# Performance work log

Measured on AMD Instinct MI355X. Metric: run time of the kernel, lower is better.

The kernel has to match this reference:

```python
import jax, jax.numpy as jnp
import numpy as np

DIM_H = 384
EPS = 0.5
HID = 768
NN = 3   # num_normal_labels (B,I,O)
NL = 7   # num_labels (O, B/I x POS/NEG/NEU)


def _make_w_trans():
    # ote_vocab: B=0, I=1, O=2 ; ts_vocab: O=0, B-POS=1, B-NEG=2, B-NEU=3, I-POS=4, I-NEG=5, I-NEU=6
    W = np.zeros((NN, NL), dtype=np.float32)
    W[0, 1] = W[0, 2] = W[0, 3] = 1.0 / 3.0  # B -> B-*
    W[1, 4] = W[1, 5] = W[1, 6] = 1.0 / 3.0  # I -> I-*
    W[2, 0] = 1.0                            # O -> O
    return jnp.asarray(W)


def setup_inputs() -> dict:
    key = jax.random.key(0)
    ks = jax.random.split(key, 16)
    B, S = 32, 512
    s = 0.02
    inp = {
        'x': jax.random.normal(ks[0], (B, S, HID), jnp.float32),
        'attention_mask': jnp.ones((B, S), jnp.int32),
        'labels': jax.random.randint(ks[1], (B, S), 0, NL, jnp.int32),
        'labels_normal': jax.random.randint(ks[2], (B, S), 0, NN, jnp.int32),
        'W_fc_normal': jax.random.normal(ks[3], (HID, NN), jnp.float32) * s,
        'b_fc_normal': jnp.zeros((NN,), jnp.float32),
        'w_ih_f': jax.random.normal(ks[4], (4 * DIM_H, HID), jnp.float32) * s,
        'w_hh_f': jax.random.normal(ks[5], (4 * DIM_H, DIM_H), jnp.float32) * s,
        'b_f': jnp.zeros((4 * DIM_H,), jnp.float32),
        'w_ih_b': jax.random.normal(ks[6], (4 * DIM_H, HID), jnp.float32) * s,
        'w_hh_b': jax.random.normal(ks[7], (4 * DIM_H, DIM_H), jnp.float32) * s,
        'b_b': jnp.zeros((4 * DIM_H,), jnp.float32),
        'W_gate': jax.random.uniform(ks[8], (2 * DIM_H, 2 * DIM_H), jnp.float32, -0.2, 0.2),
        'W_fc_upper': jax.random.normal(ks[9], (2 * DIM_H, NL), jnp.float32) * s,
        'b_fc_upper': jnp.zeros((NL,), jnp.float32),
        'W_trans': _make_w_trans(),
    }
    return inp


def _lstm_dir(xs, w_ih, w_hh, b):
    # xs: [S, B, HID] time-major; PyTorch gate order i,f,g,o
    B = xs.shape[1]
    pre = jnp.einsum('sbh,gh->sbg', xs, w_ih) + b  # precompute input projections

    def step(carry, p_t):
        h, c = carry
        g = p_t + h @ w_hh.T
        i, f, gg, o = jnp.split(g, 4, axis=-1)
        c = jax.nn.sigmoid(f) * c + jax.nn.sigmoid(i) * jnp.tanh(gg)
        h = jax.nn.sigmoid(o) * jnp.tanh(c)
        return (h, c), h

    init = (jnp.zeros((B, DIM_H), xs.dtype), jnp.zeros((B, DIM_H), xs.dtype))
    _, hs = jax.lax.scan(step, init, pre)
    return hs  # [S, B, DIM_H]


def _masked_ce(logits, labels, mask):
    logp = jax.nn.log_softmax(logits, axis=-1)
    nll = -jnp.take_along_axis(logp, labels[..., None].astype(jnp.int32), axis=-1)[..., 0]
    m = mask.astype(logits.dtype)
    return jnp.sum(nll * m) / jnp.sum(m)


def reference(x, attention_mask, labels, labels_normal, W_fc_normal, b_fc_normal,
              w_ih_f, w_hh_f, b_f, w_ih_b, w_hh_b, b_b, W_gate,
              W_fc_upper, b_fc_upper, W_trans):
    z_t = x @ W_fc_normal + b_fc_normal                      # [B,S,NN]
    loss = _masked_ce(z_t, labels_normal, attention_mask)

    xs = jnp.transpose(x, (1, 0, 2))                         # [S,B,HID]
    hf = _lstm_dir(xs, w_ih_f, w_hh_f, b_f)
    hb = _lstm_dir(xs[::-1], w_ih_b, w_hh_b, b_b)[::-1]
    h_s = jnp.concatenate([hf, hb], axis=-1)                 # [S,B,2*DIM_H]

    # gated highway recurrence: gates depend only on h_s -> batched matmul + linear scan
    g = jax.nn.sigmoid(h_s @ W_gate)                         # [S,B,768]

    def gate_step(h_prev, inp):
        ht, gt = inp
        h = gt * ht + (1.0 - gt) * h_prev
        return h, h

    _, rest = jax.lax.scan(gate_step, h_s[0], (h_s[1:], g[1:]))
    h_tilde = jnp.concatenate([h_s[:1], rest], axis=0)       # [S,B,768]
    h_tilde = jnp.transpose(h_tilde, (1, 0, 2))              # [B,S,768]; dropout = identity (eval)

    z_s = h_tilde @ W_fc_upper + b_fc_upper                  # [B,S,NL]
    p = jax.nn.softmax(z_t, axis=-1)
    alpha = EPS * jnp.sum(p * p, axis=-1, keepdims=True)     # [B,S,1]
    z_s_prime = z_t @ W_trans                                # [B,S,NL]
    z_s_tilde = z_s_prime * alpha + z_s * (1.0 - alpha)

    loss = loss + _masked_ce(z_s_tilde, labels, attention_mask)
    return loss, z_s_tilde
```

## Files before the change

kernel.cpp:

```cpp
#include <hip/hip_runtime.h>

#define B_SZ   32
#define S_LEN  512
#define HID    768
#define DH     384
#define G4     1536
#define NPOS   16384
#define EPS_C  0.5f
#define NCH    24576
#define CHK    64
#define NCHK   8

typedef _Float16 h2 __attribute__((ext_vector_type(2)));
typedef short bf16x8 __attribute__((ext_vector_type(8)));
typedef float f32x4 __attribute__((ext_vector_type(4)));

static __device__ __forceinline__ float sigm(float x) { return 1.0f / (1.0f + __expf(-x)); }
static __device__ __forceinline__ float tanh_fast(float x) {
    return 1.0f - 2.0f / (__expf(2.0f * x) + 1.0f);
}

static __device__ __forceinline__ unsigned short f2bf(float f) {
    union { float f; unsigned u; } v; v.f = f;
    unsigned r = v.u + 0x7FFF + ((v.u >> 16) & 1);
    return (unsigned short)(r >> 16);
}
static __device__ __forceinline__ float bf2f(unsigned short u) {
    union { unsigned u; float f; } v; v.u = ((unsigned)u) << 16; return v.f;
}

static __device__ __forceinline__ float wred(float v) {
#pragma unroll
    for (int off = 32; off > 0; off >>= 1) v += __shfl_down(v, off, 64);
    return v;
}

static __device__ __forceinline__ float dot2acc(h2 a, h2 b, float c) {
#if __has_builtin(__builtin_amdgcn_fdot2)
    return __builtin_amdgcn_fdot2(a, b, c, false);
#else
    return c + (float)a.x * (float)b.x + (float)a.y * (float)b.y;
#endif
}

static __device__ __forceinline__ h2 hcast(unsigned u) { return __builtin_bit_cast(h2, u); }

template <int CTRL>
static __device__ __forceinline__ float qperm_add(float v) {
#if __has_builtin(__builtin_amdgcn_mov_dpp)
    int o = __builtin_amdgcn_mov_dpp(__builtin_bit_cast(int, v), CTRL, 0xF, 0xF, true);
    return v + __builtin_bit_cast(float, o);
#else
    return v + __shfl_xor(v, (CTRL == 0xB1) ? 1 : 2, 64);
#endif
}

__global__ void wprep(const float* __restrict__ wf, const float* __restrict__ wb,
                      unsigned* __restrict__ wpk) {
    int gid = blockIdx.x * 256 + threadIdx.x;
    int d = (gid >= 294912) ? 1 : 0;
    int j = gid - d * 294912;
    const float* src = d ? wb : wf;
    _Float16 a = (_Float16)src[2 * j];
    _Float16 b = (_Float16)src[2 * j + 1];
    unsigned pa = __builtin_bit_cast(unsigned short, a);
    unsigned pb = __builtin_bit_cast(unsigned short, b);
    wpk[(size_t)d * 294912 + j] = pa | (pb << 16);
}

__global__ __launch_bounds__(256) void cast_bf16(
    const float* __restrict__ src, unsigned short* __restrict__ dst, int n4) {
    int i = blockIdx.x * 256 + threadIdx.x;
    if (i >= n4) return;
    float4 v = *(const float4*)(src + (size_t)i * 4);
    ushort4 o;
    o.x = f2bf(v.x); o.y = f2bf(v.y); o.z = f2bf(v.z); o.w = f2bf(v.w);
    *(ushort4*)(dst + (size_t)i * 4) = o;
}

__global__ __launch_bounds__(256) void wgt_prep(
    const float* __restrict__ Wg, unsigned short* __restrict__ Wgt) {
    int i = blockIdx.x * 256 + threadIdx.x;
    int k = i / 768, n = i - k * 768;
    Wgt[(size_t)n * 768 + k] = f2bf(Wg[i]);
}

__global__ __launch_bounds__(256) void zt_kernel(
    const float* __restrict__ x, const int* __restrict__ amask,
    const int* __restrict__ labn, const float* __restrict__ Wfc,
    const float* __restrict__ bfc, const float* __restrict__ Wtr,
    float* __restrict__ alpha, float* __restrict__ zsp,
    float* __restrict__ p0, float* __restrict__ p2) {
    const int gid  = blockIdx.x * blockDim.x + threadIdx.x;
    const int pos  = gid >> 6, lane = gid & 63, wv = threadIdx.x >> 6;
    __shared__ float r0[4], r2[4];
    const float* xp = x + (size_t)pos * HID;
    float a0 = 0.f, a1 = 0.f, a2 = 0.f;
#pragma unroll
    for (int j = 0; j < 12; ++j) {
        int k = lane + (j << 6);
        float xv = xp[k];
        a0 += xv * Wfc[k * 3 + 0];
        a1 += xv * Wfc[k * 3 + 1];
        a2 += xv * Wfc[k * 3 + 2];
    }
    a0 = wred(a0); a1 = wred(a1); a2 = wred(a2);
    if (lane == 0) {
        float z0 = a0 + bfc[0], z1 = a1 + bfc[1], z2 = a2 + bfc[2];
        float mx = fmaxf(z0, fmaxf(z1, z2));
        float e0 = __expf(z0 - mx), e1 = __expf(z1 - mx), e2 = __expf(z2 - mx);
        float se = e0 + e1 + e2;
        float m  = (float)amask[pos];
        int  lab = labn[pos];
        float zl = (lab == 0) ? z0 : ((lab == 1) ? z1 : z2);
        r0[wv] = (mx + __logf(se) - zl) * m;
        r2[wv] = m;
        float q0 = e0 / se, q1 = e1 / se, q2 = e2 / se;
        alpha[pos] = EPS_C * (q0 * q0 + q1 * q1 + q2 * q2);
#pragma unroll
        for (int cc = 0; cc < 7; ++cc)
            zsp[(size_t)pos * 7 + cc] = z0 * Wtr[cc] + z1 * Wtr[7 + cc] + z2 * Wtr[14 + cc];
    }
    __syncthreads();
    if (threadIdx.x == 0) {
        p0[blockIdx.x] = r0[0] + r0[1] + r0[2] + r0[3];
        p2[blockIdx.x] = r2[0] + r2[1] + r2[2] + r2[3];
    }
}

__global__ __launch_bounds__(256) void gemm_mfma(
    const unsigned short* __restrict__ A, const unsigned short* __restrict__ B,
    const float* __restrict__ bias, void* __restrict__ Cout,
    int M, int N, int K, int mode) {
    __shared__ __align__(16) unsigned short As[128][40];
    __shared__ __align__(16) unsigned short Bs[128][40];
    const int tid = threadIdx.x;
    const int m0 = blockIdx.y * 128, n0 = blockIdx.x * 128;
    const int wave = tid >> 6, lane = tid & 63;
    const int wm = (wave & 1) * 64, wn = (wave >> 1) * 64;
    const int lm = lane & 15, quad = lane >> 4;
    f32x4 acc[4][4] = {};

    for (int k0 = 0; k0 < K; k0 += 32) {
#pragma unroll
        for (int r = 0; r < 2; ++r) {
            int seg = tid + r * 256;
            int row = seg >> 2, c16 = (seg & 3) << 3;
            uint4 va = *(const uint4*)(A + (size_t)(m0 + row) * K + k0 + c16);
            *(uint4*)&As[row][c16] = va;
            uint4 vb = *(const uint4*)(B + (size_t)(n0 + row) * K + k0 + c16);
            *(uint4*)&Bs[row][c16] = vb;
        }
        __syncthreads();
        bf16x8 af[4], bfr[4];
#pragma unroll
        for (int i = 0; i < 4; ++i) {
            af[i]  = *(const bf16x8*)&As[wm + i * 16 + lm][quad * 8];
            bfr[i] = *(const bf16x8*)&Bs[wn + i * 16 + lm][quad * 8];
        }
#pragma unroll
        for (int mi = 0; mi < 4; ++mi)
#pragma unroll
            for (int ni = 0; ni < 4; ++ni)
                acc[mi][ni] = __builtin_amdgcn_mfma_f32_16x16x32_bf16(
                    af[mi], bfr[ni], acc[mi][ni], 0, 0, 0);
        __syncthreads();
    }

    const int rbase = quad * 4;
#pragma unroll
    for (int mi = 0; mi < 4; ++mi) {
#pragma unroll
        for (int ni = 0; ni < 4; ++ni) {
            const int col = n0 + wn + ni * 16 + lm;
            const float bv = (mode == 0) ? bias[col] : 0.0f;
#pragma unroll
            for (int r = 0; r < 4; ++r) {
                const int row = m0 + wm + mi * 16 + rbase + r;
                float v = acc[mi][ni][r];
                if (mode == 0)
                    ((unsigned short*)Cout)[(size_t)row * N + col] = f2bf(v + bv);
                else
                    ((unsigned short*)Cout)[(size_t)row * N + col] = f2bf(sigm(v));
            }
        }
    }
}

#define DOT8(W, H, A0, A1) { \
    A0 = dot2acc(hcast(W.x), hcast(H.x), A0); \
    A1 = dot2acc(hcast(W.y), hcast(H.y), A1); \
    A0 = dot2acc(hcast(W.z), hcast(H.z), A0); \
    A1 = dot2acc(hcast(W.w), hcast(H.w), A1); }

__global__ __launch_bounds__(768)
__attribute__((amdgpu_waves_per_eu(3, 3)))
void lstm_scan9(
    const unsigned* __restrict__ wpk,
    const unsigned short* __restrict__ pre,
    unsigned short* __restrict__ h_sb,
    unsigned long long* __restrict__ hx64) {
    const int blk   = blockIdx.x;
    const int chain = blk & 63;
    const int rp    = blk >> 6;
    const int d = chain >> 5, b = chain & 31;
    const int tid = threadIdx.x;
    const int j = tid >> 2;
    const int p = tid & 3;
    const int ga = j / 96, ua = j - ga * 96;
    const int base = rp * 96;
    const int Ga = ga * 384 + base + ua;

    __shared__ __align__(16) _Float16 lh16[2][384];
    __shared__ float    lpreV[384];
    __shared__ unsigned lpreT[384];

    const uint4* wqA = (const uint4*)wpk + ((size_t)d * 1536 + Ga) * 48 + p * 12;
    const uint4* wqB = wqA + 36864;
    const uint4 wa0 = wqA[0], wa1 = wqA[1], wa2  = wqA[2],  wa3  = wqA[3],
                wa4 = wqA[4], wa5 = wqA[5], wa6  = wqA[6],  wa7  = wqA[7],
                wa8 = wqA[8], wa9 = wqA[9], wa10 = wqA[10], wa11 = wqA[11];
    const uint4 wb0 = wqB[0], wb1 = wqB[1], wb2  = wqB[2],  wb3  = wqB[3],
                wb4 = wqB[4], wb5 = wqB[5], wb6  = wqB[6],  wb7  = wqB[7],
                wb8 = wqB[8], wb9 = wqB[9], wb10 = wqB[10], wb11 = wqB[11];

    const unsigned short* prb =
        pre + ((size_t)d * B_SZ + b) * S_LEN * G4 + Ga + ((p == 1) ? 768 : 0);

    float c = 0.0f;

    for (int s = 0; s < S_LEN; ++s) {
        const int t  = d ? (S_LEN - 1 - s) : s;
        const int lb = s & 1;
        float prev = 0.0f;
        if (p < 2) prev = bf2f(prb[(size_t)t * G4]);

        if (s == 0) {
            if (tid < 384) { lh16[0][tid] = (_Float16)0.0f; lpreT[tid] = 0xFFFFFFFFu; }
        } else if (tid < 288) {
            const int uu = tid + (tid >= base ? 96 : 0);
            const unsigned long long* srcp =
                hx64 + ((size_t)((s - 1) & 1) * 64 + chain) * 384 + uu;
            unsigned long long v =
                __hip_atomic_load(srcp, __ATOMIC_RELAXED, __HIP_MEMORY_SCOPE_AGENT);
            while ((unsigned)(v >> 32) != (unsigned)(s - 1)) {
                __builtin_amdgcn_s_sleep(1);
                v = __hip_atomic_load(srcp, __ATOMIC_RELAXED, __HIP_MEMORY_SCOPE_AGENT);
            }
            lh16[lb][uu] = (_Float16)__builtin_bit_cast(float, (unsigned)v);
        }
        __syncthreads();

        {
            const uint4* hq = (const uint4*)&lh16[lb][0] + p * 12;
            const uint4 hv0 = hq[0], hv1 = hq[1], hv2  = hq[2],  hv3  = hq[3],
                        hv4 = hq[4], hv5 = hq[5], hv6  = hq[6],  hv7  = hq[7],
                        hv8 = hq[8], hv9 = hq[9], hv10 = hq[10], hv11 = hq[11];
            float a0 = 0.f, a1 = 0.f, b0 = 0.f, b1 = 0.f;
            DOT8(wa0, hv0, a0, a1)  DOT8(wa1, hv1, a0, a1)  DOT8(wa2,  hv2,  a0, a1)
            DOT8(wa3, hv3, a0, a1)  DOT8(wa4, hv4, a0, a1)  DOT8(wa5,  hv5,  a0, a1)
            DOT8(wa6, hv6, a0, a1)  DOT8(wa7, hv7, a0, a1)  DOT8(wa8,  hv8,  a0, a1)
            DOT8(wa9, hv9, a0, a1)  DOT8(wa10, hv10, a0, a1) DOT8(wa11, hv11, a0, a1)
            DOT8(wb0, hv0, b0, b1)  DOT8(wb1, hv1, b0, b1)  DOT8(wb2,  hv2,  b0, b1)
            DOT8(wb3, hv3, b0, b1)  DOT8(wb4, hv4, b0, b1)  DOT8(wb5,  hv5,  b0, b1)
            DOT8(wb6, hv6, b0, b1)  DOT8(wb7, hv7, b0, b1)  DOT8(wb8,  hv8,  b0, b1)
            DOT8(wb9, hv9, b0, b1)  DOT8(wb10, hv10, b0, b1) DOT8(wb11, hv11, b0, b1)
            float sa = a0 + a1, sb = b0 + b1;
            sa = qperm_add<0xB1>(sa); sa = qperm_add<0x4E>(sa);
            sb = qperm_add<0xB1>(sb); sb = qperm_add<0x4E>(sb);
            if (p == 0) {
                lpreV[j] = sa + prev;
                __hip_atomic_store(&lpreT[j], (unsigned)s, __ATOMIC_RELEASE,
                                   __HIP_MEMORY_SCOPE_WORKGROUP);
            } else if (p == 1) {
                lpreV[j + 192] = sb + prev;
                __hip_atomic_store(&lpreT[j + 192], (unsigned)s, __ATOMIC_RELEASE,
                                   __HIP_MEMORY_SCOPE_WORKGROUP);
            }
        }

        if (tid < 96) {
            const unsigned sv = (unsigned)s;
#pragma unroll
            for (int jj = 0; jj < 4; ++jj) {
                unsigned* tp = &lpreT[jj * 96 + tid];
                while (__hip_atomic_load(tp, __ATOMIC_ACQUIRE,
                                         __HIP_MEMORY_SCOPE_WORKGROUP) != sv) {}
            }
            float gi = lpreV[tid], gf = lpreV[96 + tid];
            float gg = lpreV[192 + tid], go = lpreV[288 + tid];
            c = sigm(gf) * c + sigm(gi) * tanh_fast(gg);
            float h = sigm(go) * tanh_fast(c);
            unsigned long long v = ((unsigned long long)sv << 32)
                                 | (unsigned long long)__builtin_bit_cast(unsigned, h);
            __hip_atomic_store(hx64 + ((size_t)lb * 64 + chain) * 384 + base + tid,
                               v, __ATOMIC_RELAXED, __HIP_MEMORY_SCOPE_AGENT);
            h_sb[((size_t)t * B_SZ + b) * HID + d * DH + base + tid] = f2bf(h);
            lh16[lb ^ 1][base + tid] = (_Float16)h;
        }
    }
}

__global__ __launch_bounds__(256) void gscanA(
    const unsigned short* __restrict__ g, const unsigned short* __restrict__ hsb,
    float2* __restrict__ ab) {
    int id = blockIdx.x * 256 + threadIdx.x;
    int chunk = id / NCH, chain = id - chunk * NCH;
    int t0 = chunk * CHK;
    float A = 1.f, Bv = 0.f;
    for (int i = 0; i < CHK; ++i) {
        int t = t0 + i;
        size_t idx = (size_t)t * NCH + chain;
        float gv = bf2f(g[idx]);
        float hv = bf2f(hsb[idx]);
        float a = (t == 0) ? 0.f : (1.f - gv);
        float bb = (t == 0) ? hv : gv * hv;
        A  = a * A;
        Bv = a * Bv + bb;
    }
    ab[id] = make_float2(A, Bv);
}

__global__ __launch_bounds__(256) void gscanB(
    const float2* __restrict__ ab, float* __restrict__ cin) {
    int chain = blockIdx.x * 256 + threadIdx.x;
    float h = 0.f;
#pragma unroll
    for (int j = 0; j < NCHK; ++j) {
        cin[(size_t)j * NCH + chain] = h;
        float2 t = ab[(size_t)j * NCH + chain];
        h = t.x * h + t.y;
    }
}

__global__ __launch_bounds__(256) void gscanC(
    const unsigned short* __restrict__ g, unsigned short* __restrict__ hsb,
    const float* __restrict__ cin) {
    int id = blockIdx.x * 256 + threadIdx.x;
    int chunk = id / NCH, chain = id - chunk * NCH;
    int t0 = chunk * CHK;
    float h = cin[(size_t)chunk * NCH + chain];
    for (int i = 0; i < CHK; ++i) {
        int t = t0 + i;
        size_t idx = (size_t)t * NCH + chain;
        float gv = bf2f(g[idx]);
        float v  = bf2f(hsb[idx]);
        h = (t == 0) ? v : (gv * v + (1.f - gv) * h);
        hsb[idx] = f2bf(h);
    }
}

__global__ __launch_bounds__(256) void final_k(
    const unsigned short* __restrict__ ht, const float* __restrict__ Wup,
    const float* __restrict__ bup, const float* __restrict__ alpha,
    const float* __restrict__ zsp, const int* __restrict__ labels,
    const int* __restrict__ amask, float* __restrict__ out, float* __restrict__ p1) {
    const int gid = blockIdx.x * blockDim.x + threadIdx.x;
    const int pos = gid >> 6, lane = gid & 63, wv = threadIdx.x >> 6;
    __shared__ float r1[4];
    const int bb = pos >> 9, tt = pos & 511;
    const unsigned short* hp = ht + (size_t)tt * (B_SZ * HID) + (size_t)bb * HID;
    float acc[7] = {};
#pragma unroll
    for (int j = 0; j < 12; ++j) {
        int k = lane + (j << 6);
        float hv = bf2f(hp[k]);
        const float* wr = Wup + k * 7;
#pragma unroll
        for (int cc = 0; cc < 7; ++cc) acc[cc] += hv * wr[cc];
    }
#pragma unroll
    for (int cc = 0; cc < 7; ++cc) acc[cc] = wred(acc[cc]);
    if (lane == 0) {
        float al = alpha[pos];
        float z[7], mx = -1e30f;
#pragma unroll
        for (int cc = 0; cc < 7; ++cc) {
            float v = acc[cc] + bup[cc];
            v = zsp[(size_t)pos * 7 + cc] * al + v * (1.0f - al);
            z[cc] = v;
            mx = fmaxf(mx, v);
            out[1 + (size_t)pos * 7 + cc] = v;
        }
        float se = 0.f;
#pragma unroll
        for (int cc = 0; cc < 7; ++cc) se += __expf(z[cc] - mx);
        float lse = mx + __logf(se);
        int lab = labels[pos];
        float zl = z[0];
#pragma unroll
        for (int cc = 1; cc < 7; ++cc) if (lab == cc) zl = z[cc];
        float m = (float)amask[pos];
        r1[wv] = (lse - zl) * m;
    }
    __syncthreads();
    if (threadIdx.x == 0)
        p1[blockIdx.x] = r1[0] + r1[1] + r1[2] + r1[3];
}

__global__ __launch_bounds__(256) void loss_k(
    const float* __restrict__ p0, const float* __restrict__ p1,
    const float* __restrict__ p2, float* __restrict__ out) {
    const int tid = threadIdx.x, lane = tid & 63, wv = tid >> 6;
    __shared__ float rs[4][3];
    float s0 = 0.f, s1 = 0.f, s2 = 0.f;
    for (int i = tid; i < 4096; i += 256) {
        s0 += p0[i]; s1 += p1[i]; s2 += p2[i];
    }
    s0 = wred(s0); s1 = wred(s1); s2 = wred(s2);
    if (lane == 0) { rs[wv][0] = s0; rs[wv][1] = s1; rs[wv][2] = s2; }
    __syncthreads();
    if (tid == 0) {
        float t0 = rs[0][0] + rs[1][0] + rs[2][0] + rs[3][0];
        float t1 = rs[0][1] + rs[1][1] + rs[2][1] + rs[3][1];
        float t2 = rs[0][2] + rs[1][2] + rs[2][2] + rs[3][2];
        out[0] = t0 / t2 + t1 / t2;
    }
}

extern "C" void kernel_launch(void* const* d_in, const int* in_sizes, int n_in,
                              void* d_out, int out_size, void* d_ws, size_t ws_size,
                              hipStream_t stream) {
    const float* x     = (const float*)d_in[0];
    const int*   amask = (const int*)d_in[1];
    const int*   labels= (const int*)d_in[2];
    const int*   labn  = (const int*)d_in[3];
    const float* Wfc   = (const float*)d_in[4];
    const float* bfc   = (const float*)d_in[5];
    const float* wihf  = (const float*)d_in[6];
    const float* whhf  = (const float*)d_in[7];
    const float* bf    = (const float*)d_in[8];
    const float* wihb  = (const float*)d_in[9];
    const float* whhb  = (const float*)d_in[10];
    const float* bb    = (const float*)d_in[11];
    const float* Wg    = (const float*)d_in[12];
    const float* Wup   = (const float*)d_in[13];
    const float* bup   = (const float*)d_in[14];
    const float* Wtr   = (const float*)d_in[15];
    float* out = (float*)d_out;
    (void)in_sizes; (void)n_in; (void)out_size; (void)ws_size;

    char* ws = (char*)d_ws;
    size_t off = 0;
    auto alloc = [&](size_t bytes) -> char* {
        char* p = ws + off;
        off = (off + bytes + 255) & ~(size_t)255;
        return p;
    };
    unsigned* w16buf    = (unsigned*)alloc((size_t)2 * 1536 * 192 * 4);
    unsigned short* pre = (unsigned short*)alloc((size_t)2 * NPOS * G4 * 2);
    unsigned short* xb  = (unsigned short*)alloc((size_t)NPOS * HID * 2);
    unsigned short* wfb = (unsigned short*)alloc((size_t)G4 * HID * 2);
    unsigned short* wbb = (unsigned short*)alloc((size_t)G4 * HID * 2);
    unsigned short* wgt = (unsigned short*)alloc((size_t)HID * HID * 2);
    float* alpha        = (float*)alloc((size_t)NPOS * 4);
    float* zsp          = (float*)alloc((size_t)NPOS * 7 * 4);
    unsigned long long* hx64 = (unsigned long long*)alloc((size_t)2 * 64 * 384 * 8);
    float2* ab          = (float2*)alloc((size_t)NCHK * NCH * 8);
    float* cin          = (float*)alloc((size_t)NCHK * NCH * 4);
    float* part0        = (float*)alloc(4096 * 4);
    float* part1        = (float*)alloc(4096 * 4);
    float* part2        = (float*)alloc(4096 * 4);
    unsigned short* gbuf = (unsigned short*)pre;
    unsigned short* h_sb = xb;


    wprep<<<2304, 256, 0, stream>>>(whhf, whhb, w16buf);
    cast_bf16<<<12288, 256, 0, stream>>>(x, xb, NPOS * HID / 4);
    cast_bf16<<<1152, 256, 0, stream>>>(wihf, wfb, G4 * HID / 4);
    cast_bf16<<<1152, 256, 0, stream>>>(wihb, wbb, G4 * HID / 4);
    wgt_prep<<<2304, 256, 0, stream>>>(Wg, wgt);

    zt_kernel<<<4096, 256, 0, stream>>>(x, amask, labn, Wfc, bfc, Wtr, alpha, zsp,
                                        part0, part2);

    gemm_mfma<<<dim3(12, 128), 256, 0, stream>>>(xb, wfb, bf, pre, NPOS, G4, HID, 0);
    gemm_mfma<<<dim3(12, 128), 256, 0, stream>>>(xb, wbb, bb, pre + (size_t)NPOS * G4,
                                                 NPOS, G4, HID, 0);

    lstm_scan9<<<256, 768, 0, stream>>>(w16buf, pre, h_sb, hx64);

    gemm_mfma<<<dim3(6, 128), 256, 0, stream>>>(h_sb, wgt, nullptr, gbuf, NPOS, HID, HID, 1);

    gscanA<<<768, 256, 0, stream>>>(gbuf, h_sb, ab);
    gscanB<<<96, 256, 0, stream>>>(ab, cin);
    gscanC<<<768, 256, 0, stream>>>(gbuf, h_sb, cin);

    final_k<<<4096, 256, 0, stream>>>(h_sb, Wup, bup, alpha, zsp, labels, amask, out, part1);

    loss_k<<<1, 256, 0, stream>>>(part0, part1, part2, out);
}
```

Measured before the change: 1.368 ms.

## Give each hidden unit all four gates in one 8-lane group, removing LDS handoff

The LSTM scan kernel now assigns 8 lanes per hidden unit, with each lane computing partial dot products for all four gates (i,f,g,o) over a 48-element slice of h. The lanes reduce with DPP shifts, and lane 0 applies the cell update directly. This removes the shared-memory gate staging and the intra-workgroup spin-wait flags that the 96 update threads used. Each lane now loads four weight slices instead of two. The DPP row-shift reduction must stay correct within 8-lane groups, and the fallback path uses shfl_down.

```diff
diff --git a/kernel.cpp b/kernel.cpp
--- a/kernel.cpp
+++ b/kernel.cpp
@@ -46,13 +46,19 @@
 static __device__ __forceinline__ h2 hcast(unsigned u) { return __builtin_bit_cast(h2, u); }
 
 template <int CTRL>
-static __device__ __forceinline__ float qperm_add(float v) {
+static __device__ __forceinline__ float dpp_shl_add(float v) {
 #if __has_builtin(__builtin_amdgcn_mov_dpp)
     int o = __builtin_amdgcn_mov_dpp(__builtin_bit_cast(int, v), CTRL, 0xF, 0xF, true);
     return v + __builtin_bit_cast(float, o);
 #else
-    return v + __shfl_xor(v, (CTRL == 0xB1) ? 1 : 2, 64);
+    return v + __shfl_down(v, CTRL - 0x100, 64);
 #endif
+}
+static __device__ __forceinline__ float red8(float v) {
+    v = dpp_shl_add<0x101>(v);
+    v = dpp_shl_add<0x102>(v);
+    v = dpp_shl_add<0x104>(v);
+    return v;
 }
 
 __global__ void wprep(const float* __restrict__ wf, const float* __restrict__ wb,
@@ -195,7 +201,7 @@
 
 __global__ __launch_bounds__(768)
 __attribute__((amdgpu_waves_per_eu(3, 3)))
-void lstm_scan9(
+void lstm_scan10(
     const unsigned* __restrict__ wpk,
     const unsigned short* __restrict__ pre,
     unsigned short* __restrict__ h_sb,
@@ -205,27 +211,25 @@
     const int rp    = blk >> 6;
     const int d = chain >> 5, b = chain & 31;
     const int tid = threadIdx.x;
-    const int j = tid >> 2;
-    const int p = tid & 3;
-    const int ga = j / 96, ua = j - ga * 96;
+    const int u = tid >> 3;
+    const int p = tid & 7;
     const int base = rp * 96;
-    const int Ga = ga * 384 + base + ua;
+    const int G0 = base + u;
 
     __shared__ __align__(16) _Float16 lh16[2][384];
-    __shared__ float    lpreV[384];
-    __shared__ unsigned lpreT[384];
-
-    const uint4* wqA = (const uint4*)wpk + ((size_t)d * 1536 + Ga) * 48 + p * 12;
-    const uint4* wqB = wqA + 36864;
-    const uint4 wa0 = wqA[0], wa1 = wqA[1], wa2  = wqA[2],  wa3  = wqA[3],
-                wa4 = wqA[4], wa5 = wqA[5], wa6  = wqA[6],  wa7  = wqA[7],
-                wa8 = wqA[8], wa9 = wqA[9], wa10 = wqA[10], wa11 = wqA[11];
-    const uint4 wb0 = wqB[0], wb1 = wqB[1], wb2  = wqB[2],  wb3  = wqB[3],
-                wb4 = wqB[4], wb5 = wqB[5], wb6  = wqB[6],  wb7  = wqB[7],
-                wb8 = wqB[8], wb9 = wqB[9], wb10 = wqB[10], wb11 = wqB[11];
+
+    const uint4* wq = (const uint4*)wpk + ((size_t)d * 1536 + G0) * 48 + p * 6;
+    const uint4 wi0 = wq[0],         wi1 = wq[1],         wi2 = wq[2],
+                wi3 = wq[3],         wi4 = wq[4],         wi5 = wq[5];
+    const uint4 wf0 = wq[18432],     wf1 = wq[18433],     wf2 = wq[18434],
+                wf3 = wq[18435],     wf4 = wq[18436],     wf5 = wq[18437];
+    const uint4 wg0 = wq[36864],     wg1 = wq[36865],     wg2 = wq[36866],
+                wg3 = wq[36867],     wg4 = wq[36868],     wg5 = wq[36869];
+    const uint4 wo0 = wq[55296],     wo1 = wq[55297],     wo2 = wq[55298],
+                wo3 = wq[55299],     wo4 = wq[55300],     wo5 = wq[55301];
 
     const unsigned short* prb =
-        pre + ((size_t)d * B_SZ + b) * S_LEN * G4 + Ga + ((p == 1) ? 768 : 0);
+        pre + ((size_t)d * B_SZ + b) * S_LEN * G4 + G0 + (p & 3) * 384;
 
     float c = 0.0f;
 
@@ -233,10 +237,10 @@
         const int t  = d ? (S_LEN - 1 - s) : s;
         const int lb = s & 1;
         float prev = 0.0f;
-        if (p < 2) prev = bf2f(prb[(size_t)t * G4]);
+        if (p < 4) prev = bf2f(prb[(size_t)t * G4]);
 
         if (s == 0) {
-            if (tid < 384) { lh16[0][tid] = (_Float16)0.0f; lpreT[tid] = 0xFFFFFFFFu; }
+            if (tid < 384) lh16[0][tid] = (_Float16)0.0f;
         } else if (tid < 288) {
             const int uu = tid + (tid >= base ? 96 : 0);
             const unsigned long long* srcp =
@@ -252,51 +256,36 @@
         __syncthreads();
 
         {
-            const uint4* hq = (const uint4*)&lh16[lb][0] + p * 12;
-            const uint4 hv0 = hq[0], hv1 = hq[1], hv2  = hq[2],  hv3  = hq[3],
-                        hv4 = hq[4], hv5 = hq[5], hv6  = hq[6],  hv7  = hq[7],
-                        hv8 = hq[8], hv9 = hq[9], hv10 = hq[10], hv11 = hq[11];
-            float a0 = 0.f, a1 = 0.f, b0 = 0.f, b1 = 0.f;
-            DOT8(wa0, hv0, a0, a1)  DOT8(wa1, hv1, a0, a1)  DOT8(wa2,  hv2,  a0, a1)
-            DOT8(wa3, hv3, a0, a1)  DOT8(wa4, hv4, a0, a1)  DOT8(wa5,  hv5,  a0, a1)
-            DOT8(wa6, hv6, a0, a1)  DOT8(wa7, hv7, a0, a1)  DOT8(wa8,  hv8,  a0, a1)
-            DOT8(wa9, hv9, a0, a1)  DOT8(wa10, hv10, a0, a1) DOT8(wa11, hv11, a0, a1)
-            DOT8(wb0, hv0, b0, b1)  DOT8(wb1, hv1, b0, b1)  DOT8(wb2,  hv2,  b0, b1)
-            DOT8(wb3, hv3, b0, b1)  DOT8(wb4, hv4, b0, b1)  DOT8(wb5,  hv5,  b0, b1)
-            DOT8(wb6, hv6, b0, b1)  DOT8(wb7, hv7, b0, b1)  DOT8(wb8,  hv8,  b0, b1)
-            DOT8(wb9, hv9, b0, b1)  DOT8(wb10, hv10, b0, b1) DOT8(wb11, hv11, b0, b1)
-            float sa = a0 + a1, sb = b0 + b1;
-            sa = qperm_add<0xB1>(sa); sa = qperm_add<0x4E>(sa);
-            sb = qperm_add<0xB1>(sb); sb = qperm_add<0x4E>(sb);
+            const uint4* hq = (const uint4*)&lh16[lb][0] + p * 6;
+            const uint4 h0 = hq[0], h1 = hq[1], h2 = hq[2],
+                        h3 = hq[3], h4 = hq[4], h5 = hq[5];
+            float i0 = 0.f, i1 = 0.f, f0 = 0.f, f1 = 0.f;
+            float g0 = 0.f, g1 = 0.f, o0 = 0.f, o1 = 0.f;
+            DOT8(wi0, h0, i0, i1) DOT8(wi1, h1, i0, i1) DOT8(wi2, h2, i0, i1)
+            DOT8(wi3, h3, i0, i1) DOT8(wi4, h4, i0, i1) DOT8(wi5, h5, i0, i1)
+            DOT8(wf0, h0, f0, f1) DOT8(wf1, h1, f0, f1) DOT8(wf2, h2, f0, f1)
+            DOT8(wf3, h3, f0, f1) DOT8(wf4, h4, f0, f1) DOT8(wf5, h5, f0, f1)
+            DOT8(wg0, h0, g0, g1) DOT8(wg1, h1, g0, g1) DOT8(wg2, h2, g0, g1)
+            DOT8(wg3, h3, g0, g1) DOT8(wg4, h4, g0, g1) DOT8(wg5, h5, g0, g1)
+            DOT8(wo0, h0, o0, o1) DOT8(wo1, h1, o0, o1) DOT8(wo2, h2, o0, o1)
+            DOT8(wo3, h3, o0, o1) DOT8(wo4, h4, o0, o1) DOT8(wo5, h5, o0, o1)
+            float gi = i0 + i1, gf = f0 + f1, gg = g0 + g1, go = o0 + o1;
+            if      (p == 0) gi += prev;
+            else if (p == 1) gf += prev;
+            else if (p == 2) gg += prev;
+            else if (p == 3) go += prev;
+            gi = red8(gi); gf = red8(gf); gg = red8(gg); go = red8(go);
+
             if (p == 0) {
-                lpreV[j] = sa + prev;
-                __hip_atomic_store(&lpreT[j], (unsigned)s, __ATOMIC_RELEASE,
-                                   __HIP_MEMORY_SCOPE_WORKGROUP);
-            } else if (p == 1) {
-                lpreV[j + 192] = sb + prev;
-                __hip_atomic_store(&lpreT[j + 192], (unsigned)s, __ATOMIC_RELEASE,
-                                   __HIP_MEMORY_SCOPE_WORKGROUP);
+                c = sigm(gf) * c + sigm(gi) * tanh_fast(gg);
+                float h = sigm(go) * tanh_fast(c);
+                unsigned long long v = ((unsigned long long)(unsigned)s << 32)
+                                     | (unsigned long long)__builtin_bit_cast(unsigned, h);
+                __hip_atomic_store(hx64 + ((size_t)lb * 64 + chain) * 384 + G0,
+                                   v, __ATOMIC_RELAXED, __HIP_MEMORY_SCOPE_AGENT);
+                h_sb[((size_t)t * B_SZ + b) * HID + d * DH + G0] = f2bf(h);
+                lh16[lb ^ 1][G0] = (_Float16)h;
             }
-        }
-
-        if (tid < 96) {
-            const unsigned sv = (unsigned)s;
-#pragma unroll
-            for (int jj = 0; jj < 4; ++jj) {
-                unsigned* tp = &lpreT[jj * 96 + tid];
-                while (__hip_atomic_load(tp, __ATOMIC_ACQUIRE,
-                                         __HIP_MEMORY_SCOPE_WORKGROUP) != sv) {}
-            }
-            float gi = lpreV[tid], gf = lpreV[96 + tid];
-            float gg = lpreV[192 + tid], go = lpreV[288 + tid];
-            c = sigm(gf) * c + sigm(gi) * tanh_fast(gg);
-            float h = sigm(go) * tanh_fast(c);
-            unsigned long long v = ((unsigned long long)sv << 32)
-                                 | (unsigned long long)__builtin_bit_cast(unsigned, h);
-            __hip_atomic_store(hx64 + ((size_t)lb * 64 + chain) * 384 + base + tid,
-                               v, __ATOMIC_RELAXED, __HIP_MEMORY_SCOPE_AGENT);
-            h_sb[((size_t)t * B_SZ + b) * HID + d * DH + base + tid] = f2bf(h);
-            lh16[lb ^ 1][base + tid] = (_Float16)h;
         }
     }
 }
@@ -478,7 +467,7 @@
     gemm_mfma<<<dim3(12, 128), 256, 0, stream>>>(xb, wbb, bb, pre + (size_t)NPOS * G4,
                                                  NPOS, G4, HID, 0);
 
-    lstm_scan9<<<256, 768, 0, stream>>>(w16buf, pre, h_sb, hx64);
+    lstm_scan10<<<256, 768, 0, stream>>>(w16buf, pre, h_sb, hx64);
 
     gemm_mfma<<<dim3(6, 128), 256, 0, stream>>>(h_sb, wgt, nullptr, gbuf, NPOS, HID, HID, 1);
 
```

New measurement: 1.376 ms. Within noise of the previous version (+0.6%).
